# Kernel tuning notes

Measured on AMD Instinct MI355X. Metric: run time of the kernel, lower is better.

## Reference

```python
import jax, jax.numpy as jnp
import numpy as np

B, N, NC, C, H = 8, 1024, 64, 1024, 16
D = C // H  # head_dim = 64
SCALE = D ** -0.5


def setup_inputs() -> dict:
    key = jax.random.key(0)
    ks = jax.random.split(key, 6)
    s = 0.02
    return {
        "x": jax.random.normal(ks[0], (B, N, C), jnp.float32),
        "cond": jax.random.normal(ks[1], (B, NC, C), jnp.float32),
        "W_qkv": jax.random.normal(ks[2], (3 * C, C), jnp.float32) * s,
        "W_qkv_c": jax.random.normal(ks[3], (3 * C, C), jnp.float32) * s,
        "W_proj": jax.random.normal(ks[4], (C, C), jnp.float32) * s,
        "b_proj": jnp.zeros((C,), jnp.float32),
        "W_proj_c": jax.random.normal(ks[5], (C, C), jnp.float32) * s,
        "b_proj_c": jnp.zeros((C,), jnp.float32),
    }


def _qkv_heads(t, W):
    # t: [B, L, C] -> q, k, v each [B, H, L, D]
    b, l, c = t.shape
    qkv = (t @ W.T).reshape(b, l, 3, H, D)
    qkv = jnp.transpose(qkv, (2, 0, 3, 1, 4))  # [3, B, H, L, D]
    return qkv[0], qkv[1], qkv[2]


def reference(x, cond, W_qkv, W_qkv_c, W_proj, b_proj, W_proj_c, b_proj_c):
    q, k, v = _qkv_heads(x, W_qkv)          # [B,H,N,D]
    q_c, k_c, v_c = _qkv_heads(cond, W_qkv_c)  # [B,H,NC,D]
    # concat main-stream and cond-stream tokens along sequence axis
    q = jnp.concatenate((q, q_c), axis=-2) * SCALE  # [B,H,N+NC,D]
    k = jnp.concatenate((k, k_c), axis=-2)
    v = jnp.concatenate((v, v_c), axis=-2)
    attn = jnp.einsum("bhqd,bhkd->bhqk", q, k)  # [B,H,N+NC,N+NC]
    attn = jax.nn.softmax(attn, axis=-1)
    out = jnp.einsum("bhqk,bhkd->bhqd", attn, v)  # [B,H,N+NC,D]
    out = jnp.transpose(out, (0, 2, 1, 3)).reshape(x.shape[0], N + NC, C)
    x_out = out[:, :N] @ W_proj.T + b_proj
    cond_out = out[:, N:] @ W_proj_c.T + b_proj_c
    return (x_out, cond_out)
```

## Files before the change

kernel.cpp:

```cpp
#include <hip/hip_runtime.h>
#include <hip/hip_bf16.h>

#define LTOT 1088
#define CDIM 1024
#define NH 16
#define HD 64

typedef __attribute__((ext_vector_type(8))) short short8;
typedef __attribute__((ext_vector_type(4))) float f32x4;

__device__ __forceinline__ unsigned short f2b(float f) {
  union { float f; unsigned int u; } a; a.f = f;
  unsigned int r = a.u + 0x7FFFu + ((a.u >> 16) & 1u);
  return (unsigned short)(r >> 16);
}

__device__ __forceinline__ f32x4 mfma16(short8 a, short8 b, f32x4 c) {
  return __builtin_amdgcn_mfma_f32_16x16x32_bf16(a, b, c, 0, 0, 0);
}

#define GLL16(gsrc, ldst)                                                        \
  __builtin_amdgcn_global_load_lds(                                              \
      (const __attribute__((address_space(1))) void*)(gsrc),                     \
      (__attribute__((address_space(3))) void*)(ldst), 16, 0, 0)

__global__ __launch_bounds__(256) void cvt_kernel(const float* __restrict__ in,
                                                  unsigned short* __restrict__ out,
                                                  int n4) {
  int i = blockIdx.x * 256 + threadIdx.x;
  if (i >= n4) return;
  float4 f = ((const float4*)in)[i];
  ushort4 o;
  o.x = f2b(f.x); o.y = f2b(f.y); o.z = f2b(f.z); o.w = f2b(f.w);
  ((ushort4*)out)[i] = o;
}

__global__ __launch_bounds__(256) void gemm_qkv(
    const unsigned short* __restrict__ A, const unsigned short* __restrict__ Bw,
    unsigned short* __restrict__ qo, unsigned short* __restrict__ ko,
    unsigned short* __restrict__ vo, int bshift, int tokbase) {
  const int K = 1024;
  __shared__ __align__(16) unsigned short As[128 * 32];
  __shared__ __align__(16) unsigned short Bs[128 * 32];
  const int tid = threadIdx.x;
  const int wid = tid >> 6, lane = tid & 63;
  const int bm = blockIdx.x, bn = blockIdx.y;
  const int wm = wid >> 1, wn = wid & 1;
  const int lcol = lane & 15, lk8 = (lane >> 4) * 8;
  const int c0 = wid * 64 + lane;

  f32x4 acc[4][4];
#pragma unroll
  for (int i = 0; i < 4; ++i)
#pragma unroll
    for (int j = 0; j < 4; ++j) acc[i][j] = (f32x4){0.f, 0.f, 0.f, 0.f};

  for (int k0 = 0; k0 < K; k0 += 32) {
#pragma unroll
    for (int i = 0; i < 2; ++i) {
      int c = i * 256 + c0;
      int row = c >> 2, kc = c & 3;
      GLL16(A + (size_t)(bm * 128 + row) * K + k0 + kc * 8, &As[c * 8]);
      GLL16(Bw + (size_t)(bn * 128 + row) * K + k0 + kc * 8, &Bs[c * 8]);
    }
    __syncthreads();
    short8 af[4], bf[4];
#pragma unroll
    for (int mf = 0; mf < 4; ++mf)
      af[mf] = *(const short8*)&As[(wm * 64 + mf * 16 + lcol) * 32 + lk8];
#pragma unroll
    for (int nf = 0; nf < 4; ++nf)
      bf[nf] = *(const short8*)&Bs[(wn * 64 + nf * 16 + lcol) * 32 + lk8];
#pragma unroll
    for (int mf = 0; mf < 4; ++mf)
#pragma unroll
      for (int nf = 0; nf < 4; ++nf) acc[mf][nf] = mfma16(af[mf], bf[nf], acc[mf][nf]);
    __syncthreads();
  }

  const int which = bn >> 3;
  const int bmask = (1 << bshift) - 1;
#pragma unroll
  for (int mf = 0; mf < 4; ++mf) {
    int Rbase = bm * 128 + wm * 64 + mf * 16 + (lane >> 4) * 4;
    int b = Rbase >> bshift;
    int tok = tokbase + (Rbase & bmask);
#pragma unroll
    for (int nf = 0; nf < 4; ++nf) {
      int Cc = bn * 128 + wn * 64 + nf * 16 + lcol;
      int ch = Cc & 1023;
      int h = ch >> 6, d = ch & 63;
      size_t head = (size_t)(b * NH + h);
      if (which == 0) {
#pragma unroll
        for (int r = 0; r < 4; ++r)
          qo[(head * LTOT + tok + r) * HD + d] = f2b(acc[mf][nf][r] * 0.125f);
      } else if (which == 1) {
#pragma unroll
        for (int r = 0; r < 4; ++r)
          ko[(head * LTOT + tok + r) * HD + d] = f2b(acc[mf][nf][r]);
      } else {
        ushort4 pk;
        pk.x = f2b(acc[mf][nf][0]); pk.y = f2b(acc[mf][nf][1]);
        pk.z = f2b(acc[mf][nf][2]); pk.w = f2b(acc[mf][nf][3]);
        *(ushort4*)&vo[(head * HD + d) * LTOT + tok] = pk;
      }
    }
  }
}

__global__ __launch_bounds__(256) void attn_kernel(
    const unsigned short* __restrict__ q, const unsigned short* __restrict__ k,
    const unsigned short* __restrict__ vt, unsigned short* __restrict__ ao) {
  int bid = blockIdx.x;
  int swz = (bid & 7) * 272 + (bid >> 3);
  int head = swz / 17;
  int qt = swz - head * 17;
  int b = head >> 4, h = head & 15;
  const int tid = threadIdx.x, wid = tid >> 6, lane = tid & 63;
  const int lcol = lane & 15, lk8 = (lane >> 4) * 8;

  __shared__ __align__(16) unsigned short Ks[64 * 64];
  __shared__ __align__(16) unsigned short Vs[64 * 64];
  __shared__ __align__(16) unsigned short Ps[4][16 * 64];

  const unsigned short* qh = q + (size_t)head * LTOT * HD;
  const unsigned short* kh = k + (size_t)head * LTOT * HD;
  const unsigned short* vh = vt + (size_t)head * HD * LTOT;

  int qrow = qt * 64 + wid * 16 + lcol;
  short8 qf[2];
  qf[0] = *(const short8*)(qh + (size_t)qrow * HD + lk8);
  qf[1] = *(const short8*)(qh + (size_t)qrow * HD + 32 + lk8);

  f32x4 o[4];
#pragma unroll
  for (int i = 0; i < 4; ++i) o[i] = (f32x4){0.f, 0.f, 0.f, 0.f};
  float m_r[4] = {-1e30f, -1e30f, -1e30f, -1e30f};
  float l_r[4] = {0.f, 0.f, 0.f, 0.f};

  const int c0 = wid * 64 + lane;
  char* Pw = (char*)&Ps[wid][0];

  for (int kt = 0; kt < 17; ++kt) {
    int kv0 = kt * 64;
#pragma unroll
    for (int i = 0; i < 2; ++i) {
      int c = i * 256 + c0;
      int row = c >> 3, chk = c & 7;
      int sc = chk ^ (row & 7);
      GLL16(kh + (size_t)(kv0 + row) * HD + sc * 8, &Ks[c * 8]);
      GLL16(vh + (size_t)row * LTOT + kv0 + sc * 8, &Vs[c * 8]);
    }
    __syncthreads();

    f32x4 s[4];
#pragma unroll
    for (int nf = 0; nf < 4; ++nf) {
      int kvr = nf * 16 + lcol;
      int base = kvr * 128, xr = (kvr & 7) << 4;
      short8 kf0 = *(const short8*)((const char*)Ks + base + ((lk8 * 2) ^ xr));
      short8 kf1 = *(const short8*)((const char*)Ks + base + (((32 + lk8) * 2) ^ xr));
      f32x4 z = (f32x4){0.f, 0.f, 0.f, 0.f};
      z = mfma16(qf[0], kf0, z);
      z = mfma16(qf[1], kf1, z);
      s[nf] = z;
    }

    float fsc[4], rs[4];
#pragma unroll
    for (int r = 0; r < 4; ++r) {
      float t0 = fmaxf(fmaxf(s[0][r], s[1][r]), fmaxf(s[2][r], s[3][r]));
      t0 = fmaxf(t0, __shfl_xor(t0, 1));
      t0 = fmaxf(t0, __shfl_xor(t0, 2));
      t0 = fmaxf(t0, __shfl_xor(t0, 4));
      t0 = fmaxf(t0, __shfl_xor(t0, 8));
      float mn = fmaxf(m_r[r], t0);
      fsc[r] = __expf(m_r[r] - mn);
      m_r[r] = mn;
      rs[r] = 0.f;
    }
#pragma unroll
    for (int nf = 0; nf < 4; ++nf) {
      int kvc = nf * 16 + lcol;
#pragma unroll
      for (int r = 0; r < 4; ++r) {
        float p = __expf(s[nf][r] - m_r[r]);
        rs[r] += p;
        int qrl = (lane >> 4) * 4 + r;
        *(unsigned short*)(Pw + qrl * 128 + ((kvc * 2) ^ ((qrl & 7) << 4))) = f2b(p);
      }
    }
#pragma unroll
    for (int r = 0; r < 4; ++r) {
      float t1 = rs[r];
      t1 += __shfl_xor(t1, 1);
      t1 += __shfl_xor(t1, 2);
      t1 += __shfl_xor(t1, 4);
      t1 += __shfl_xor(t1, 8);
      l_r[r] = l_r[r] * fsc[r] + t1;
    }
#pragma unroll
    for (int nfd = 0; nfd < 4; ++nfd)
#pragma unroll
      for (int r = 0; r < 4; ++r) o[nfd][r] *= fsc[r];

    short8 pf[2];
    {
      int base = lcol * 128, xr = (lcol & 7) << 4;
      pf[0] = *(const short8*)((const char*)Pw + base + ((lk8 * 2) ^ xr));
      pf[1] = *(const short8*)((const char*)Pw + base + (((32 + lk8) * 2) ^ xr));
    }
#pragma unroll
    for (int nfd = 0; nfd < 4; ++nfd) {
      int dr = nfd * 16 + lcol;
      int base = dr * 128, xr = (dr & 7) << 4;
      short8 vf0 = *(const short8*)((const char*)Vs + base + ((lk8 * 2) ^ xr));
      short8 vf1 = *(const short8*)((const char*)Vs + base + (((32 + lk8) * 2) ^ xr));
      o[nfd] = mfma16(pf[0], vf0, o[nfd]);
      o[nfd] = mfma16(pf[1], vf1, o[nfd]);
    }
    __syncthreads();
  }

#pragma unroll
  for (int nfd = 0; nfd < 4; ++nfd) {
#pragma unroll
    for (int r = 0; r < 4; ++r) {
      int tok = qt * 64 + wid * 16 + (lane >> 4) * 4 + r;
      float val = o[nfd][r] / l_r[r];
      ao[((size_t)b * LTOT + tok) * CDIM + h * HD + nfd * 16 + lcol] = f2b(val);
    }
  }
}

__global__ __launch_bounds__(256) void gemm_proj(
    const unsigned short* __restrict__ A, const unsigned short* __restrict__ Bw,
    const float* __restrict__ bias, float* __restrict__ out, int bshift, int tokbase) {
  const int K = 1024;
  __shared__ __align__(16) unsigned short As[128 * 32];
  __shared__ __align__(16) unsigned short Bs[128 * 32];
  const int tid = threadIdx.x;
  const int wid = tid >> 6, lane = tid & 63;
  const int bm = blockIdx.x, bn = blockIdx.y;
  const int wm = wid >> 1, wn = wid & 1;
  const int lcol = lane & 15, lk8 = (lane >> 4) * 8;
  const int c0 = wid * 64 + lane;
  const int bmask = (1 << bshift) - 1;

  f32x4 acc[4][4];
#pragma unroll
  for (int i = 0; i < 4; ++i)
#pragma unroll
    for (int j = 0; j < 4; ++j) acc[i][j] = (f32x4){0.f, 0.f, 0.f, 0.f};

  for (int k0 = 0; k0 < K; k0 += 32) {
#pragma unroll
    for (int i = 0; i < 2; ++i) {
      int c = i * 256 + c0;
      int row = c >> 2, kc = c & 3;
      int R = bm * 128 + row;
      size_t arow = (size_t)(R >> bshift) * LTOT + tokbase + (R & bmask);
      GLL16(A + arow * K + k0 + kc * 8, &As[c * 8]);
      GLL16(Bw + (size_t)(bn * 128 + row) * K + k0 + kc * 8, &Bs[c * 8]);
    }
    __syncthreads();
    short8 af[4], bf[4];
#pragma unroll
    for (int mf = 0; mf < 4; ++mf)
      af[mf] = *(const short8*)&As[(wm * 64 + mf * 16 + lcol) * 32 + lk8];
#pragma unroll
    for (int nf = 0; nf < 4; ++nf)
      bf[nf] = *(const short8*)&Bs[(wn * 64 + nf * 16 + lcol) * 32 + lk8];
#pragma unroll
    for (int mf = 0; mf < 4; ++mf)
#pragma unroll
      for (int nf = 0; nf < 4; ++nf) acc[mf][nf] = mfma16(af[mf], bf[nf], acc[mf][nf]);
    __syncthreads();
  }

#pragma unroll
  for (int mf = 0; mf < 4; ++mf) {
    int Rbase = bm * 128 + wm * 64 + mf * 16 + (lane >> 4) * 4;
#pragma unroll
    for (int nf = 0; nf < 4; ++nf) {
      int Cc = bn * 128 + wn * 64 + nf * 16 + lcol;
      float bv = bias[Cc];
#pragma unroll
      for (int r = 0; r < 4; ++r)
        out[(size_t)(Rbase + r) * 1024 + Cc] = acc[mf][nf][r] + bv;
    }
  }
}

extern "C" void kernel_launch(void* const* d_in, const int* in_sizes, int n_in,
                              void* d_out, int out_size, void* d_ws, size_t ws_size,
                              hipStream_t stream) {
  (void)in_sizes; (void)n_in; (void)out_size; (void)ws_size;
  const float* x     = (const float*)d_in[0];
  const float* cond  = (const float*)d_in[1];
  const float* Wqkv  = (const float*)d_in[2];
  const float* Wqkvc = (const float*)d_in[3];
  const float* Wp    = (const float*)d_in[4];
  const float* bp    = (const float*)d_in[5];
  const float* Wpc   = (const float*)d_in[6];
  const float* bpc   = (const float*)d_in[7];
  float* out = (float*)d_out;

  char* ws = (char*)d_ws;
  unsigned short* xb      = (unsigned short*)(ws + 0);
  unsigned short* condb   = (unsigned short*)(ws + 16777216);
  unsigned short* wqkvb   = (unsigned short*)(ws + 17825792);
  unsigned short* wqkvcb  = (unsigned short*)(ws + 24117248);
  unsigned short* wprojb  = (unsigned short*)(ws + 30408704);
  unsigned short* wprojcb = (unsigned short*)(ws + 32505856);
  unsigned short* qb      = (unsigned short*)(ws + 34603008);
  unsigned short* kbuf    = (unsigned short*)(ws + 52428800);
  unsigned short* vbuf    = (unsigned short*)(ws + 70254592);
  unsigned short* aob     = (unsigned short*)(ws + 88080384);

  cvt_kernel<<<8192, 256, 0, stream>>>(x, xb, 2097152);
  cvt_kernel<<<512, 256, 0, stream>>>(cond, condb, 131072);
  cvt_kernel<<<3072, 256, 0, stream>>>(Wqkv, wqkvb, 786432);
  cvt_kernel<<<3072, 256, 0, stream>>>(Wqkvc, wqkvcb, 786432);
  cvt_kernel<<<1024, 256, 0, stream>>>(Wp, wprojb, 262144);
  cvt_kernel<<<1024, 256, 0, stream>>>(Wpc, wprojcb, 262144);

  gemm_qkv<<<dim3(64, 24), 256, 0, stream>>>(xb, wqkvb, qb, kbuf, vbuf, 10, 0);
  gemm_qkv<<<dim3(4, 24), 256, 0, stream>>>(condb, wqkvcb, qb, kbuf, vbuf, 6, 1024);

  attn_kernel<<<2176, 256, 0, stream>>>(qb, kbuf, vbuf, aob);

  gemm_proj<<<dim3(64, 8), 256, 0, stream>>>(aob, wprojb, bp, out, 10, 0);
  gemm_proj<<<dim3(4, 8), 256, 0, stream>>>(aob, wprojcb, bpc, out + 8388608, 6, 1024);
}
```

Measured before the change: 394.6 us.

## Double-buffer attention K/V tiles, transpose score MFMA, and merge conversion launches

Attention now double-buffers the K/V shared-memory tiles, prefetching the next tile while the current one is computed, and uses explicit vmcnt waits with raw barriers. It swaps the QK^T MFMA operands so each lane holds one query row, which makes the softmax reductions cheaper and lets P be written with packed bf16 stores. The rescale factor is broadcast by shuffle, and priority hints surround the MFMA blocks. The six fp32-to-bf16 conversion launches are merged into one kernel to reduce launch overhead. In exchange, attention uses twice the shared memory for K/V, which may lower occupancy.

```diff
diff --git a/kernel.cpp b/kernel.cpp
--- a/kernel.cpp
+++ b/kernel.cpp
@@ -24,15 +24,26 @@
       (const __attribute__((address_space(1))) void*)(gsrc),                     \
       (__attribute__((address_space(3))) void*)(ldst), 16, 0, 0)
 
-__global__ __launch_bounds__(256) void cvt_kernel(const float* __restrict__ in,
-                                                  unsigned short* __restrict__ out,
-                                                  int n4) {
+__global__ __launch_bounds__(256) void cvt_all(
+    const float* __restrict__ s0, const float* __restrict__ s1,
+    const float* __restrict__ s2, const float* __restrict__ s3,
+    const float* __restrict__ s4, const float* __restrict__ s5,
+    unsigned short* __restrict__ d0, unsigned short* __restrict__ d1,
+    unsigned short* __restrict__ d2, unsigned short* __restrict__ d3,
+    unsigned short* __restrict__ d4, unsigned short* __restrict__ d5) {
   int i = blockIdx.x * 256 + threadIdx.x;
-  if (i >= n4) return;
-  float4 f = ((const float4*)in)[i];
-  ushort4 o;
-  o.x = f2b(f.x); o.y = f2b(f.y); o.z = f2b(f.z); o.w = f2b(f.w);
-  ((ushort4*)out)[i] = o;
+  const float* s; unsigned short* d; int off;
+  if (i < 2097152)      { s = s0; d = d0; off = 0; }
+  else if (i < 2228224) { s = s1; d = d1; off = 2097152; }
+  else if (i < 3014656) { s = s2; d = d2; off = 2228224; }
+  else if (i < 3801088) { s = s3; d = d3; off = 3014656; }
+  else if (i < 4063232) { s = s4; d = d4; off = 3801088; }
+  else                  { s = s5; d = d5; off = 4063232; }
+  int j = i - off;
+  float4 f = ((const float4*)s)[j];
+  ushort4 o4;
+  o4.x = f2b(f.x); o4.y = f2b(f.y); o4.z = f2b(f.z); o4.w = f2b(f.w);
+  ((ushort4*)d)[j] = o4;
 }
 
 __global__ __launch_bounds__(256) void gemm_qkv(
@@ -118,10 +129,10 @@
   int qt = swz - head * 17;
   int b = head >> 4, h = head & 15;
   const int tid = threadIdx.x, wid = tid >> 6, lane = tid & 63;
-  const int lcol = lane & 15, lk8 = (lane >> 4) * 8;
-
-  __shared__ __align__(16) unsigned short Ks[64 * 64];
-  __shared__ __align__(16) unsigned short Vs[64 * 64];
+  const int lcol = lane & 15, grp = lane >> 4, lk8 = grp * 8;
+
+  __shared__ __align__(16) unsigned short Ks[2][64 * 64];
+  __shared__ __align__(16) unsigned short Vs[2][64 * 64];
   __shared__ __align__(16) unsigned short Ps[4][16 * 64];
 
   const unsigned short* qh = q + (size_t)head * LTOT * HD;
@@ -136,99 +147,122 @@
   f32x4 o[4];
 #pragma unroll
   for (int i = 0; i < 4; ++i) o[i] = (f32x4){0.f, 0.f, 0.f, 0.f};
-  float m_r[4] = {-1e30f, -1e30f, -1e30f, -1e30f};
-  float l_r[4] = {0.f, 0.f, 0.f, 0.f};
+  float m_r = -1e30f, l_r = 0.f;
 
   const int c0 = wid * 64 + lane;
   char* Pw = (char*)&Ps[wid][0];
 
+#define STAGE(bb, kt_)                                                           \
+  do {                                                                           \
+    int kv0_ = (kt_) * 64;                                                       \
+    _Pragma("unroll")                                                            \
+    for (int i_ = 0; i_ < 2; ++i_) {                                             \
+      int c_ = i_ * 256 + c0;                                                    \
+      int row_ = c_ >> 3, chk_ = c_ & 7;                                         \
+      int sc_ = chk_ ^ (row_ & 7);       \
+      GLL16(kh + (size_t)(kv0_ + row_) * HD + sc_ * 8, &Ks[bb][c_ * 8]);         \
+      GLL16(vh + (size_t)row_ * LTOT + kv0_ + sc_ * 8, &Vs[bb][c_ * 8]);         \
+    }                                                                            \
+  } while (0)
+
+  STAGE(0, 0);
+
   for (int kt = 0; kt < 17; ++kt) {
-    int kv0 = kt * 64;
-#pragma unroll
-    for (int i = 0; i < 2; ++i) {
-      int c = i * 256 + c0;
-      int row = c >> 3, chk = c & 7;
-      int sc = chk ^ (row & 7);
-      GLL16(kh + (size_t)(kv0 + row) * HD + sc * 8, &Ks[c * 8]);
-      GLL16(vh + (size_t)row * LTOT + kv0 + sc * 8, &Vs[c * 8]);
-    }
-    __syncthreads();
-
-    f32x4 s[4];
+    int cur = kt & 1;
+    if (kt < 16) {
+      STAGE(cur ^ 1, kt + 1);
+      asm volatile("s_waitcnt vmcnt(4)" ::: "memory");
+    } else {
+      asm volatile("s_waitcnt vmcnt(0)" ::: "memory");
+    }
+    __builtin_amdgcn_s_barrier();
+
+    const char* Kb = (const char*)&Ks[cur][0];
+    const char* Vb = (const char*)&Vs[cur][0];
+
+    f32x4 st[4];
+    __builtin_amdgcn_s_setprio(1);
 #pragma unroll
     for (int nf = 0; nf < 4; ++nf) {
       int kvr = nf * 16 + lcol;
       int base = kvr * 128, xr = (kvr & 7) << 4;
-      short8 kf0 = *(const short8*)((const char*)Ks + base + ((lk8 * 2) ^ xr));
-      short8 kf1 = *(const short8*)((const char*)Ks + base + (((32 + lk8) * 2) ^ xr));
+      short8 kf0 = *(const short8*)(Kb + base + ((lk8 * 2) ^ xr));
+      short8 kf1 = *(const short8*)(Kb + base + (((32 + lk8) * 2) ^ xr));
       f32x4 z = (f32x4){0.f, 0.f, 0.f, 0.f};
-      z = mfma16(qf[0], kf0, z);
-      z = mfma16(qf[1], kf1, z);
-      s[nf] = z;
-    }
-
-    float fsc[4], rs[4];
+      z = mfma16(kf0, qf[0], z);
+      z = mfma16(kf1, qf[1], z);
+      st[nf] = z;
+    }
+    __builtin_amdgcn_s_setprio(0);
+
+    float tmax = st[0][0];
+#pragma unroll
+    for (int nf = 0; nf < 4; ++nf)
+#pragma unroll
+      for (int r = 0; r < 4; ++r) tmax = fmaxf(tmax, st[nf][r]);
+    tmax = fmaxf(tmax, __shfl_xor(tmax, 16));
+    tmax = fmaxf(tmax, __shfl_xor(tmax, 32));
+    float mn = fmaxf(m_r, tmax);
+    float fsc = __expf(m_r - mn);
+    m_r = mn;
+
+    float p[4][4];
+    float psum = 0.f;
+#pragma unroll
+    for (int nf = 0; nf < 4; ++nf)
+#pragma unroll
+      for (int r = 0; r < 4; ++r) {
+        p[nf][r] = __expf(st[nf][r] - mn);
+        psum += p[nf][r];
+      }
+#pragma unroll
+    for (int nf = 0; nf < 4; ++nf) {
+      unsigned r01, r23;
+      asm("v_cvt_pk_bf16_f32 %0, %1, %2" : "=v"(r01) : "v"(p[nf][0]), "v"(p[nf][1]));
+      asm("v_cvt_pk_bf16_f32 %0, %1, %2" : "=v"(r23) : "v"(p[nf][2]), "v"(p[nf][3]));
+      uint2 pk; pk.x = r01; pk.y = r23;
+      *(uint2*)(Pw + ((lcol * 128 + nf * 32 + grp * 8) ^ ((lcol & 7) << 4))) = pk;
+    }
+    psum += __shfl_xor(psum, 16);
+    psum += __shfl_xor(psum, 32);
+    l_r = l_r * fsc + psum;
+
 #pragma unroll
     for (int r = 0; r < 4; ++r) {
-      float t0 = fmaxf(fmaxf(s[0][r], s[1][r]), fmaxf(s[2][r], s[3][r]));
-      t0 = fmaxf(t0, __shfl_xor(t0, 1));
-      t0 = fmaxf(t0, __shfl_xor(t0, 2));
-      t0 = fmaxf(t0, __shfl_xor(t0, 4));
-      t0 = fmaxf(t0, __shfl_xor(t0, 8));
-      float mn = fmaxf(m_r[r], t0);
-      fsc[r] = __expf(m_r[r] - mn);
-      m_r[r] = mn;
-      rs[r] = 0.f;
-    }
-#pragma unroll
-    for (int nf = 0; nf < 4; ++nf) {
-      int kvc = nf * 16 + lcol;
-#pragma unroll
-      for (int r = 0; r < 4; ++r) {
-        float p = __expf(s[nf][r] - m_r[r]);
-        rs[r] += p;
-        int qrl = (lane >> 4) * 4 + r;
-        *(unsigned short*)(Pw + qrl * 128 + ((kvc * 2) ^ ((qrl & 7) << 4))) = f2b(p);
-      }
-    }
-#pragma unroll
-    for (int r = 0; r < 4; ++r) {
-      float t1 = rs[r];
-      t1 += __shfl_xor(t1, 1);
-      t1 += __shfl_xor(t1, 2);
-      t1 += __shfl_xor(t1, 4);
-      t1 += __shfl_xor(t1, 8);
-      l_r[r] = l_r[r] * fsc[r] + t1;
-    }
-#pragma unroll
-    for (int nfd = 0; nfd < 4; ++nfd)
-#pragma unroll
-      for (int r = 0; r < 4; ++r) o[nfd][r] *= fsc[r];
-
-    short8 pf[2];
+      float fb = __shfl(fsc, grp * 4 + r);
+      o[0][r] *= fb; o[1][r] *= fb; o[2][r] *= fb; o[3][r] *= fb;
+    }
+
+    short8 pf0, pf1;
     {
       int base = lcol * 128, xr = (lcol & 7) << 4;
-      pf[0] = *(const short8*)((const char*)Pw + base + ((lk8 * 2) ^ xr));
-      pf[1] = *(const short8*)((const char*)Pw + base + (((32 + lk8) * 2) ^ xr));
-    }
+      pf0 = *(const short8*)(Pw + base + ((lk8 * 2) ^ xr));
+      pf1 = *(const short8*)(Pw + base + ((64 + lk8 * 2) ^ xr));
+    }
+    __builtin_amdgcn_s_setprio(1);
 #pragma unroll
     for (int nfd = 0; nfd < 4; ++nfd) {
       int dr = nfd * 16 + lcol;
       int base = dr * 128, xr = (dr & 7) << 4;
-      short8 vf0 = *(const short8*)((const char*)Vs + base + ((lk8 * 2) ^ xr));
-      short8 vf1 = *(const short8*)((const char*)Vs + base + (((32 + lk8) * 2) ^ xr));
-      o[nfd] = mfma16(pf[0], vf0, o[nfd]);
-      o[nfd] = mfma16(pf[1], vf1, o[nfd]);
-    }
-    __syncthreads();
-  }
-
+      short8 vf0 = *(const short8*)(Vb + base + ((lk8 * 2) ^ xr));
+      short8 vf1 = *(const short8*)(Vb + base + (((32 + lk8) * 2) ^ xr));
+      o[nfd] = mfma16(pf0, vf0, o[nfd]);
+      o[nfd] = mfma16(pf1, vf1, o[nfd]);
+    }
+    __builtin_amdgcn_s_setprio(0);
+    __builtin_amdgcn_s_barrier();
+  }
+#undef STAGE
+
+  float lb[4];
+#pragma unroll
+  for (int r = 0; r < 4; ++r) lb[r] = __shfl(l_r, grp * 4 + r);
 #pragma unroll
   for (int nfd = 0; nfd < 4; ++nfd) {
 #pragma unroll
     for (int r = 0; r < 4; ++r) {
-      int tok = qt * 64 + wid * 16 + (lane >> 4) * 4 + r;
-      float val = o[nfd][r] / l_r[r];
+      int tok = qt * 64 + wid * 16 + grp * 4 + r;
+      float val = o[nfd][r] / lb[r];
       ao[((size_t)b * LTOT + tok) * CDIM + h * HD + nfd * 16 + lcol] = f2b(val);
     }
   }
@@ -319,12 +353,8 @@
   unsigned short* vbuf    = (unsigned short*)(ws + 70254592);
   unsigned short* aob     = (unsigned short*)(ws + 88080384);
 
-  cvt_kernel<<<8192, 256, 0, stream>>>(x, xb, 2097152);
-  cvt_kernel<<<512, 256, 0, stream>>>(cond, condb, 131072);
-  cvt_kernel<<<3072, 256, 0, stream>>>(Wqkv, wqkvb, 786432);
-  cvt_kernel<<<3072, 256, 0, stream>>>(Wqkvc, wqkvcb, 786432);
-  cvt_kernel<<<1024, 256, 0, stream>>>(Wp, wprojb, 262144);
-  cvt_kernel<<<1024, 256, 0, stream>>>(Wpc, wprojcb, 262144);
+  cvt_all<<<16896, 256, 0, stream>>>(x, cond, Wqkv, Wqkvc, Wp, Wpc,
+                                     xb, condb, wqkvb, wqkvcb, wprojb, wprojcb);
 
   gemm_qkv<<<dim3(64, 24), 256, 0, stream>>>(xb, wqkvb, qb, kbuf, vbuf, 10, 0);
   gemm_qkv<<<dim3(4, 24), 256, 0, stream>>>(condb, wqkvcb, qb, kbuf, vbuf, 6, 1024);
```

Result: faster. 336.1 us (-14.8%).
